# Performance work log

Hardware: AMD Instinct MI355X
Metric: run time of the kernel (lower is better)

## Reference

```python
import jax, jax.numpy as jnp
import numpy as np
from jax import lax

T, H, W = 2048, 128, 160


def setup_inputs() -> dict:
    key = jax.random.key(0)
    k1, = jax.random.split(key, 1)
    batch_x = jax.random.uniform(k1, (T, 1, H, W), dtype=jnp.float32)
    # params = [close, open, dhot] / 255 (defaults 1, 5, 8)
    params = jnp.array([1.0, 5.0, 8.0], dtype=jnp.float32) / 255.0
    HT0 = jnp.zeros((H, W), dtype=jnp.float32)
    LT0 = jnp.zeros((H, W), dtype=jnp.float32)
    # ConvTranspose2d(1,1,3,padding=1) with constant weight ones/(3**2/2) = 2/9;
    # symmetric kernel + padding=1 transposed conv == SAME-padded standard conv.
    kernel = jnp.full((1, 1, 3, 3), 2.0 / 9.0, dtype=jnp.float32)
    return {"batch_x": batch_x, "params": params, "HT0": HT0, "LT0": LT0, "kernel": kernel}


def reference(batch_x, params, HT0, LT0, kernel):
    d_close, d_open, d_hot = params[0], params[1], params[2]

    def step(carry, x):
        HT, LT = carry
        img = x[0]  # (H, W)
        # hot scores computed against *pre-update* thresholds
        tmpH_hot = jax.nn.sigmoid((img - HT - d_hot) * 500.0)
        tmpH = (img - HT) > 0
        HT = jnp.where(tmpH, HT + d_open, HT - d_close)
        tmpL_hot = jax.nn.sigmoid((LT - img - d_hot) * 500.0)
        tmpL = (LT - img) > 0
        LT = jnp.where(tmpL, LT - d_open, LT + d_close)
        return (HT, LT), tmpH_hot + tmpL_hot

    _, hot = lax.scan(step, (HT0, LT0), batch_x)  # hot: (T, H, W)

    # DiffErosion: relu(1 - conv(1 - x)) with SAME padding, batched over frames
    where_zero = (1.0 - hot)[:, None, :, :]  # (T, 1, H, W)
    sub = lax.conv_general_dilated(
        where_zero, kernel, window_strides=(1, 1), padding="SAME",
        dimension_numbers=("NCHW", "OIHW", "NCHW"))
    return jax.nn.relu(1.0 - sub)  # (T, 1, H, W)
```

## Files before the change

kernel.cpp:

```cpp
#include <hip/hip_runtime.h>


#define TILE_W 16
#define TILE_H 16
#define IN_W 14
#define IN_H 14
#define BUF 8
#define PRE 32

constexpr int T_FRAMES = 2048;
constexpr int H_IMG = 128;
constexpr int W_IMG = 160;
constexpr int HW = H_IMG * W_IMG;
constexpr int SNAP = 128;
constexpr int NSNAP = T_FRAMES / SNAP - 1;
constexpr size_t WS_NEEDED = (size_t)NSNAP * HW * sizeof(float2);
constexpr float C1 = 721.3475204444817f;

__device__ __forceinline__ float dpp_from_left(float v) {
    return __int_as_float(__builtin_amdgcn_update_dpp(0, __float_as_int(v), 0x111, 0xF, 0xF, true));
}
__device__ __forceinline__ float dpp_from_right(float v) {
    return __int_as_float(__builtin_amdgcn_update_dpp(0, __float_as_int(v), 0x101, 0xF, 0xF, true));
}

__global__ __launch_bounds__(64)
void svs_scan(const float* __restrict__ x, const float* __restrict__ params,
              const float* __restrict__ HT0, const float* __restrict__ LT0,
              float2* __restrict__ snap)
{
    const int pix = (int)blockIdx.x * 64 + (int)threadIdx.x;
    const float dC = params[0];
    const float dO = params[1];

    float HT = HT0[pix];
    float LT = LT0[pix];
    const float* xp = x + pix;

    float va[PRE], vb[PRE];
    #pragma unroll
    for (int i = 0; i < PRE; ++i) va[i] = xp[i * HW];

    for (int t = 0; t < T_FRAMES; t += 2 * PRE) {
        #pragma unroll
        for (int i = 0; i < PRE; ++i) vb[i] = xp[(t + PRE + i) * HW];
        #pragma unroll
        for (int i = 0; i < PRE; ++i) {
            const float img = va[i];
            HT = ((img - HT) > 0.0f) ? (HT + dO) : (HT - dC);
            LT = ((LT - img) > 0.0f) ? (LT - dO) : (LT + dC);
        }
        if (((t + PRE) & (SNAP - 1)) == 0) {
            const int k = (t + PRE) / SNAP;
            if (k <= NSNAP) snap[(k - 1) * HW + pix] = make_float2(HT, LT);
        }
        if (t + 2 * PRE < T_FRAMES) {
            #pragma unroll
            for (int i = 0; i < PRE; ++i) va[i] = xp[(t + 2 * PRE + i) * HW];
        }
        #pragma unroll
        for (int i = 0; i < PRE; ++i) {
            const float img = vb[i];
            HT = ((img - HT) > 0.0f) ? (HT + dO) : (HT - dC);
            LT = ((LT - img) > 0.0f) ? (LT - dO) : (LT + dC);
        }
        if (((t + 2 * PRE) & (SNAP - 1)) == 0) {
            const int k = (t + 2 * PRE) / SNAP;
            if (k <= NSNAP) snap[(k - 1) * HW + pix] = make_float2(HT, LT);
        }
    }
}

__global__ __launch_bounds__(256)
void svs_compute(const float* __restrict__ x, const float* __restrict__ params,
                 const float* __restrict__ HT0, const float* __restrict__ LT0,
                 const float* __restrict__ kern, const float2* __restrict__ snap,
                 float* __restrict__ out)
{
    const int lin = (int)blockIdx.x + 12 * (int)blockIdx.y + 120 * (int)blockIdx.z;
    const int w   = (lin & 7) * 240 + (lin >> 3);
    const int bx  = w % 12;
    const int by  = (w / 12) % 10;
    const int slice = w / 120;

    const int tx = threadIdx.x & 15;
    const int ty = threadIdx.x >> 4;
    const int gx = bx * IN_W + tx - 1;
    const int gy = by * IN_H + ty - 1;
    const int t0 = slice * SNAP;

    const bool valid = (gx >= 0) & (gx < W_IMG) & (gy >= 0) & (gy < H_IMG);
    const int cx = min(max(gx, 0), W_IMG - 1);
    const int cy = min(max(gy, 0), H_IMG - 1);
    const int pix = cy * W_IMG + cx;

    const float dC   = params[0];
    const float dO   = params[1];
    const float dHot = params[2];
    const float kw   = kern[4];
    const float c0   = dHot * C1;

    float HT, LT;
    if (slice == 0) {
        HT = valid ? HT0[pix] : 0.0f;
        LT = valid ? LT0[pix] : 0.0f;
    } else {
        const float2 s = snap[(slice - 1) * HW + pix];
        HT = valid ? s.x : 0.0f;
        LT = valid ? s.y : 0.0f;
    }

    __shared__ float sm[BUF][TILE_H][TILE_W + 1];

    const bool doOut = (tx >= 1) & (tx <= IN_W) & (ty >= 1) & (ty <= IN_H) & valid;
    const int ym = max(ty - 1, 0);
    const int yp = min(ty + 1, TILE_H - 1);
    const float* xp = x + pix;
    float* op = out + pix;

    for (int tb = t0; tb < t0 + SNAP; tb += BUF) {
        float v[BUF], hot[BUF];
        #pragma unroll
        for (int i = 0; i < BUF; ++i) v[i] = xp[(tb + i) * HW];
        #pragma unroll
        for (int i = 0; i < BUF; ++i) {
            const float img = v[i];
            const float aH = img - HT;
            const float eH = __builtin_amdgcn_exp2f(fmaf(aH, -C1, c0));
            const float hH = __builtin_amdgcn_rcpf(1.0f + eH);
            HT = (aH > 0.0f) ? (HT + dO) : (HT - dC);
            const float aL = LT - img;
            const float eL = __builtin_amdgcn_exp2f(fmaf(aL, -C1, c0));
            const float hL = __builtin_amdgcn_rcpf(1.0f + eL);
            LT = (aL > 0.0f) ? (LT - dO) : (LT + dC);
            hot[i] = valid ? (hH + hL) : 1.0f;
            sm[i][ty][tx] = hot[i];
        }
        __syncthreads();
        #pragma unroll
        for (int i = 0; i < BUF; ++i) {
            const float r0 = sm[i][ym][tx];
            const float r1 = sm[i][yp][tx];
            const float vs = r0 + hot[i] + r1;
            const float S  = vs + dpp_from_left(vs) + dpp_from_right(vs);
            float o = fmaf(S, kw, -1.0f);
            o = fmaxf(o, 0.0f);
            if (doOut) op[(tb + i) * HW] = o;
        }
        __syncthreads();
    }
}

#define NCHUNK 8
constexpr int CHUNK = T_FRAMES / NCHUNK;

__global__ __launch_bounds__(256)
void svs_fused(const float* __restrict__ x, const float* __restrict__ params,
               const float* __restrict__ HT0, const float* __restrict__ LT0,
               const float* __restrict__ kern, float* __restrict__ out)
{
    const int tx = threadIdx.x & 15;
    const int ty = threadIdx.x >> 4;
    const int gx = (int)blockIdx.x * IN_W + tx - 1;
    const int gy = (int)blockIdx.y * IN_H + ty - 1;
    const int chunk = (NCHUNK - 1) - (int)blockIdx.z;

    const bool valid = (gx >= 0) & (gx < W_IMG) & (gy >= 0) & (gy < H_IMG);
    const int cx = min(max(gx, 0), W_IMG - 1);
    const int cy = min(max(gy, 0), H_IMG - 1);
    const int pix = cy * W_IMG + cx;

    const float dC   = params[0];
    const float dO   = params[1];
    const float dHot = params[2];
    const float kw   = kern[4];

    float HT = valid ? HT0[pix] : 0.0f;
    float LT = valid ? LT0[pix] : 0.0f;

    const float* xp = x + pix;
    const int t0 = chunk * CHUNK;

    for (int t = 0; t < t0; t += BUF) {
        float v[BUF];
        #pragma unroll
        for (int i = 0; i < BUF; ++i) v[i] = xp[(t + i) * HW];
        #pragma unroll
        for (int i = 0; i < BUF; ++i) {
            const float img = v[i];
            HT = ((img - HT) > 0.0f) ? (HT + dO) : (HT - dC);
            LT = ((LT - img) > 0.0f) ? (LT - dO) : (LT + dC);
        }
    }

    __shared__ float sm[BUF][TILE_H][TILE_W + 1];
    const bool doOut = (tx >= 1) & (tx <= IN_W) & (ty >= 1) & (ty <= IN_H) & valid;
    const int ym = max(ty - 1, 0);
    const int yp = min(ty + 1, TILE_H - 1);
    const float c0 = dHot * C1;
    float* op = out + pix;

    for (int tb = t0; tb < t0 + CHUNK; tb += BUF) {
        float v[BUF], hot[BUF];
        #pragma unroll
        for (int i = 0; i < BUF; ++i) v[i] = xp[(tb + i) * HW];
        #pragma unroll
        for (int i = 0; i < BUF; ++i) {
            const float img = v[i];
            const float aH = img - HT;
            const float eH = __builtin_amdgcn_exp2f(fmaf(aH, -C1, c0));
            const float hH = __builtin_amdgcn_rcpf(1.0f + eH);
            HT = (aH > 0.0f) ? (HT + dO) : (HT - dC);
            const float aL = LT - img;
            const float eL = __builtin_amdgcn_exp2f(fmaf(aL, -C1, c0));
            const float hL = __builtin_amdgcn_rcpf(1.0f + eL);
            LT = (aL > 0.0f) ? (LT - dO) : (LT + dC);
            hot[i] = valid ? (hH + hL) : 1.0f;
            sm[i][ty][tx] = hot[i];
        }
        __syncthreads();
        #pragma unroll
        for (int i = 0; i < BUF; ++i) {
            const float r0 = sm[i][ym][tx];
            const float r1 = sm[i][yp][tx];
            const float vs = r0 + hot[i] + r1;
            const float S  = vs + dpp_from_left(vs) + dpp_from_right(vs);
            float o = fmaf(S, kw, -1.0f);
            o = fmaxf(o, 0.0f);
            if (doOut) op[(tb + i) * HW] = o;
        }
        __syncthreads();
    }
}

extern "C" void kernel_launch(void* const* d_in, const int* in_sizes, int n_in,
                              void* d_out, int out_size, void* d_ws, size_t ws_size,
                              hipStream_t stream) {
    const float* x      = (const float*)d_in[0];
    const float* params = (const float*)d_in[1];
    const float* HT0p   = (const float*)d_in[2];
    const float* LT0p   = (const float*)d_in[3];
    const float* kern   = (const float*)d_in[4];
    float* out = (float*)d_out;

    if (ws_size >= WS_NEEDED) {
        float2* snap = (float2*)d_ws;
        svs_scan<<<dim3(HW / 64), dim3(64), 0, stream>>>(x, params, HT0p, LT0p, snap);
        dim3 grid2((W_IMG + IN_W - 1) / IN_W,
                   (H_IMG + IN_H - 1) / IN_H,
                   T_FRAMES / SNAP);
        svs_compute<<<grid2, dim3(256), 0, stream>>>(x, params, HT0p, LT0p, kern, snap, out);
    } else {
        dim3 grid((W_IMG + IN_W - 1) / IN_W, (H_IMG + IN_H - 1) / IN_H, NCHUNK);
        svs_fused<<<grid, dim3(256), 0, stream>>>(x, params, HT0p, LT0p, kern, out);
    }
}
```

Measured before the change: 161.9 us.

## Deepen scan prefetch to four batches, halve snapshot interval, reorder shared layout

The threshold-scan kernel now keeps four 32-frame register batches in flight instead of two, refilling each batch right after it is consumed, so more loads are outstanding per thread. The kernel is limited to one block per SIMD via launch bounds. The snapshot interval becomes a template parameter and drops to 64 frames when workspace allows, which doubles the number of compute blocks and halves each block's serial replay, at the cost of writing more snapshots. The shared-memory tile is reindexed as [row][frame][col] to change how the stencil reads map to banks.

```diff
diff --git a/kernel.cpp b/kernel.cpp
--- a/kernel.cpp
+++ b/kernel.cpp
@@ -6,16 +6,17 @@
 #define IN_W 14
 #define IN_H 14
 #define BUF 8
-#define PRE 32
+#define B32 32
 
 constexpr int T_FRAMES = 2048;
 constexpr int H_IMG = 128;
 constexpr int W_IMG = 160;
 constexpr int HW = H_IMG * W_IMG;
-constexpr int SNAP = 128;
-constexpr int NSNAP = T_FRAMES / SNAP - 1;
-constexpr size_t WS_NEEDED = (size_t)NSNAP * HW * sizeof(float2);
 constexpr float C1 = 721.3475204444817f;
+
+constexpr size_t ws_needed(int snap) {
+    return (size_t)(T_FRAMES / snap - 1) * HW * sizeof(float2);
+}
 
 __device__ __forceinline__ float dpp_from_left(float v) {
     return __int_as_float(__builtin_amdgcn_update_dpp(0, __float_as_int(v), 0x111, 0xF, 0xF, true));
@@ -24,7 +25,27 @@
     return __int_as_float(__builtin_amdgcn_update_dpp(0, __float_as_int(v), 0x101, 0xF, 0xF, true));
 }
 
-__global__ __launch_bounds__(64)
+#define ISSUE_BATCH(V, F)                          \
+    _Pragma("unroll")                              \
+    for (int i = 0; i < B32; ++i) V[i] = xp[((F) + i) * HW];
+
+#define COMP_BATCH(V)                              \
+    _Pragma("unroll")                              \
+    for (int i = 0; i < B32; ++i) {                \
+        const float img = V[i];                    \
+        HT = ((img - HT) > 0.0f) ? (HT + dO) : (HT - dC); \
+        LT = ((LT - img) > 0.0f) ? (LT - dO) : (LT + dC); \
+    }
+
+#define SNAPSHOT(F)                                \
+    if (((F) % SNAP_) == 0) {                      \
+        const int k = (F) / SNAP_ - 1;             \
+        if (k < T_FRAMES / SNAP_ - 1)              \
+            snap[k * HW + pix] = make_float2(HT, LT); \
+    }
+
+template <int SNAP_>
+__global__ __launch_bounds__(64, 1)
 void svs_scan(const float* __restrict__ x, const float* __restrict__ params,
               const float* __restrict__ HT0, const float* __restrict__ LT0,
               float2* __restrict__ snap)
@@ -37,48 +58,38 @@
     float LT = LT0[pix];
     const float* xp = x + pix;
 
-    float va[PRE], vb[PRE];
-    #pragma unroll
-    for (int i = 0; i < PRE; ++i) va[i] = xp[i * HW];
-
-    for (int t = 0; t < T_FRAMES; t += 2 * PRE) {
-        #pragma unroll
-        for (int i = 0; i < PRE; ++i) vb[i] = xp[(t + PRE + i) * HW];
-        #pragma unroll
-        for (int i = 0; i < PRE; ++i) {
-            const float img = va[i];
-            HT = ((img - HT) > 0.0f) ? (HT + dO) : (HT - dC);
-            LT = ((LT - img) > 0.0f) ? (LT - dO) : (LT + dC);
-        }
-        if (((t + PRE) & (SNAP - 1)) == 0) {
-            const int k = (t + PRE) / SNAP;
-            if (k <= NSNAP) snap[(k - 1) * HW + pix] = make_float2(HT, LT);
-        }
-        if (t + 2 * PRE < T_FRAMES) {
-            #pragma unroll
-            for (int i = 0; i < PRE; ++i) va[i] = xp[(t + 2 * PRE + i) * HW];
-        }
-        #pragma unroll
-        for (int i = 0; i < PRE; ++i) {
-            const float img = vb[i];
-            HT = ((img - HT) > 0.0f) ? (HT + dO) : (HT - dC);
-            LT = ((LT - img) > 0.0f) ? (LT - dO) : (LT + dC);
-        }
-        if (((t + 2 * PRE) & (SNAP - 1)) == 0) {
-            const int k = (t + 2 * PRE) / SNAP;
-            if (k <= NSNAP) snap[(k - 1) * HW + pix] = make_float2(HT, LT);
-        }
-    }
-}
-
+    float v0[B32], v1[B32], v2[B32], v3[B32];
+    ISSUE_BATCH(v0, 0)
+    ISSUE_BATCH(v1, B32)
+    ISSUE_BATCH(v2, 2 * B32)
+    ISSUE_BATCH(v3, 3 * B32)
+
+    for (int t = 0; t < T_FRAMES; t += 4 * B32) {
+        const bool more = (t + 4 * B32) < T_FRAMES;
+        COMP_BATCH(v0)
+        if (more) { ISSUE_BATCH(v0, t + 4 * B32) }
+        COMP_BATCH(v1)
+        SNAPSHOT(t + 2 * B32)
+        if (more) { ISSUE_BATCH(v1, t + 5 * B32) }
+        COMP_BATCH(v2)
+        if (more) { ISSUE_BATCH(v2, t + 6 * B32) }
+        COMP_BATCH(v3)
+        SNAPSHOT(t + 4 * B32)
+        if (more) { ISSUE_BATCH(v3, t + 7 * B32) }
+    }
+}
+
+template <int SNAP_>
 __global__ __launch_bounds__(256)
 void svs_compute(const float* __restrict__ x, const float* __restrict__ params,
                  const float* __restrict__ HT0, const float* __restrict__ LT0,
                  const float* __restrict__ kern, const float2* __restrict__ snap,
                  float* __restrict__ out)
 {
+    constexpr int NSLICE_ = T_FRAMES / SNAP_;
+    constexpr int TOTAL_ = 120 * NSLICE_;
     const int lin = (int)blockIdx.x + 12 * (int)blockIdx.y + 120 * (int)blockIdx.z;
-    const int w   = (lin & 7) * 240 + (lin >> 3);
+    const int w   = (lin & 7) * (TOTAL_ / 8) + (lin >> 3);
     const int bx  = w % 12;
     const int by  = (w / 12) % 10;
     const int slice = w / 120;
@@ -87,7 +98,7 @@
     const int ty = threadIdx.x >> 4;
     const int gx = bx * IN_W + tx - 1;
     const int gy = by * IN_H + ty - 1;
-    const int t0 = slice * SNAP;
+    const int t0 = slice * SNAP_;
 
     const bool valid = (gx >= 0) & (gx < W_IMG) & (gy >= 0) & (gy < H_IMG);
     const int cx = min(max(gx, 0), W_IMG - 1);
@@ -110,7 +121,7 @@
         LT = valid ? s.y : 0.0f;
     }
 
-    __shared__ float sm[BUF][TILE_H][TILE_W + 1];
+    __shared__ float sm[TILE_H][BUF][TILE_W + 1];
 
     const bool doOut = (tx >= 1) & (tx <= IN_W) & (ty >= 1) & (ty <= IN_H) & valid;
     const int ym = max(ty - 1, 0);
@@ -118,7 +129,7 @@
     const float* xp = x + pix;
     float* op = out + pix;
 
-    for (int tb = t0; tb < t0 + SNAP; tb += BUF) {
+    for (int tb = t0; tb < t0 + SNAP_; tb += BUF) {
         float v[BUF], hot[BUF];
         #pragma unroll
         for (int i = 0; i < BUF; ++i) v[i] = xp[(tb + i) * HW];
@@ -134,13 +145,13 @@
             const float hL = __builtin_amdgcn_rcpf(1.0f + eL);
             LT = (aL > 0.0f) ? (LT - dO) : (LT + dC);
             hot[i] = valid ? (hH + hL) : 1.0f;
-            sm[i][ty][tx] = hot[i];
-        }
-        __syncthreads();
-        #pragma unroll
-        for (int i = 0; i < BUF; ++i) {
-            const float r0 = sm[i][ym][tx];
-            const float r1 = sm[i][yp][tx];
+            sm[ty][i][tx] = hot[i];
+        }
+        __syncthreads();
+        #pragma unroll
+        for (int i = 0; i < BUF; ++i) {
+            const float r0 = sm[ym][i][tx];
+            const float r1 = sm[yp][i][tx];
             const float vs = r0 + hot[i] + r1;
             const float S  = vs + dpp_from_left(vs) + dpp_from_right(vs);
             float o = fmaf(S, kw, -1.0f);
@@ -193,7 +204,7 @@
         }
     }
 
-    __shared__ float sm[BUF][TILE_H][TILE_W + 1];
+    __shared__ float sm[TILE_H][BUF][TILE_W + 1];
     const bool doOut = (tx >= 1) & (tx <= IN_W) & (ty >= 1) & (ty <= IN_H) & valid;
     const int ym = max(ty - 1, 0);
     const int yp = min(ty + 1, TILE_H - 1);
@@ -216,13 +227,13 @@
             const float hL = __builtin_amdgcn_rcpf(1.0f + eL);
             LT = (aL > 0.0f) ? (LT - dO) : (LT + dC);
             hot[i] = valid ? (hH + hL) : 1.0f;
-            sm[i][ty][tx] = hot[i];
-        }
-        __syncthreads();
-        #pragma unroll
-        for (int i = 0; i < BUF; ++i) {
-            const float r0 = sm[i][ym][tx];
-            const float r1 = sm[i][yp][tx];
+            sm[ty][i][tx] = hot[i];
+        }
+        __syncthreads();
+        #pragma unroll
+        for (int i = 0; i < BUF; ++i) {
+            const float r0 = sm[ym][i][tx];
+            const float r1 = sm[yp][i][tx];
             const float vs = r0 + hot[i] + r1;
             const float S  = vs + dpp_from_left(vs) + dpp_from_right(vs);
             float o = fmaf(S, kw, -1.0f);
@@ -243,13 +254,16 @@
     const float* kern   = (const float*)d_in[4];
     float* out = (float*)d_out;
 
-    if (ws_size >= WS_NEEDED) {
+    if (ws_size >= ws_needed(64)) {
         float2* snap = (float2*)d_ws;
-        svs_scan<<<dim3(HW / 64), dim3(64), 0, stream>>>(x, params, HT0p, LT0p, snap);
-        dim3 grid2((W_IMG + IN_W - 1) / IN_W,
-                   (H_IMG + IN_H - 1) / IN_H,
-                   T_FRAMES / SNAP);
-        svs_compute<<<grid2, dim3(256), 0, stream>>>(x, params, HT0p, LT0p, kern, snap, out);
+        svs_scan<64><<<dim3(HW / 64), dim3(64), 0, stream>>>(x, params, HT0p, LT0p, snap);
+        svs_compute<64><<<dim3(12, 10, T_FRAMES / 64), dim3(256), 0, stream>>>(
+            x, params, HT0p, LT0p, kern, snap, out);
+    } else if (ws_size >= ws_needed(128)) {
+        float2* snap = (float2*)d_ws;
+        svs_scan<128><<<dim3(HW / 64), dim3(64), 0, stream>>>(x, params, HT0p, LT0p, snap);
+        svs_compute<128><<<dim3(12, 10, T_FRAMES / 128), dim3(256), 0, stream>>>(
+            x, params, HT0p, LT0p, kern, snap, out);
     } else {
         dim3 grid((W_IMG + IN_W - 1) / IN_W, (H_IMG + IN_H - 1) / IN_H, NCHUNK);
         svs_fused<<<grid, dim3(256), 0, stream>>>(x, params, HT0p, LT0p, kern, out);
```

After: 153.0 us. 1.06x faster.
